# Performance work log

Measured on AMD Instinct MI355X. Metric: run time of the kernel, lower is better.

Reference implementation:

```python
import jax, jax.numpy as jnp
import numpy as np


def setup_inputs() -> dict:
    key = jax.random.key(0)
    ks = jax.random.split(key, 5)
    B, T, C = 2, 2048, 1024
    x = jax.random.normal(ks[0], (B, T, C), dtype=jnp.float32)
    Wqkv = jax.random.normal(ks[1], (C, 3 * C), dtype=jnp.float32) * (C ** -0.5)
    bqkv = jax.random.normal(ks[2], (3 * C,), dtype=jnp.float32) * 0.02
    Wproj = jax.random.normal(ks[3], (C, C), dtype=jnp.float32) * (C ** -0.5)
    bproj = jax.random.normal(ks[4], (C,), dtype=jnp.float32) * 0.02
    return {"x": x, "Wqkv": Wqkv, "bqkv": bqkv, "Wproj": Wproj, "bproj": bproj}


def reference(x, Wqkv, bqkv, Wproj, bproj):
    B, T, C = x.shape
    n_head = 16
    hd = C // n_head
    x_proj = x @ Wqkv + bqkv  # [B, T, 3C]
    # NOTE: source reshapes (B, T, C) -> (B, n_head, T, hd) directly (no transpose);
    # we replicate that exactly for faithfulness.
    q = x_proj[:, :, :C].reshape(B, n_head, T, hd)
    k = x_proj[:, :, C:2 * C].reshape(B, n_head, T, hd)
    v = x_proj[:, :, 2 * C:].reshape(B, n_head, T, hd)
    att = jnp.einsum('bhtd,bhsd->bhts', q, k) * (1.0 / jnp.sqrt(jnp.float32(hd)))
    causal = jnp.tril(jnp.ones((T, T), dtype=bool))  # True where allowed
    att = jnp.where(causal, att, jnp.float32(-jnp.inf))
    att = jax.nn.softmax(att, axis=-1)
    y = att @ v  # [B, H, T, hd]
    y = jnp.transpose(y, (0, 2, 1, 3)).reshape(B, T, C)
    return y @ Wproj + bproj
```

## Files before the change

### kernel.cpp

```cpp
#include <hip/hip_runtime.h>
#include <hip/hip_bf16.h>
#include <stdint.h>

typedef __hip_bfloat16 bf16;
typedef __attribute__((ext_vector_type(8))) short bf16x8;
typedef __attribute__((ext_vector_type(4))) float f32x4;

__device__ __forceinline__ bf16x8 ldsv8(const bf16* p) { return *(const bf16x8*)p; }

__device__ __forceinline__ short bf_bits(float f) {
  union { bf16 h; short s; } u; u.h = __float2bfloat16(f); return u.s;
}

#define ASYNC16(ldsdst, gsrc)                                                  \
  __builtin_amdgcn_global_load_lds(                                            \
      (const __attribute__((address_space(1))) void*)(gsrc),                   \
      (__attribute__((address_space(3))) void*)(ldsdst), 16, 0, 0)

__device__ __forceinline__ bool is_bf16(const void* p) {
  const uint32_t* w = (const uint32_t*)p;
  int cnt = 0;
#pragma unroll 8
  for (int i = 0; i < 64; ++i) {
    uint32_t e = (w[i] >> 7) & 0xffu;
    cnt += (e >= 100u && e <= 150u) ? 1 : 0;
  }
  return cnt >= 40;
}

__device__ __forceinline__ float load_f32(const void* p, size_t idx, bool b16) {
  return b16 ? __bfloat162float(((const bf16*)p)[idx]) : ((const float*)p)[idx];
}

__global__ __launch_bounds__(256) void cvt_k(const float* __restrict__ in,
                                             bf16* __restrict__ out) {
  size_t i = (size_t)blockIdx.x * 256 + threadIdx.x;
  const float4 f0 = ((const float4*)in)[i * 2];
  const float4 f1 = ((const float4*)in)[i * 2 + 1];
  bf16x8 pk = {bf_bits(f0.x), bf_bits(f0.y), bf_bits(f0.z), bf_bits(f0.w),
               bf_bits(f1.x), bf_bits(f1.y), bf_bits(f1.z), bf_bits(f1.w)};
  ((bf16x8*)out)[i] = pk;
}

__global__ __launch_bounds__(256) void cvtT_k(const void* __restrict__ in,
                                              bf16* __restrict__ out,
                                              int R, int Ccols) {
  __shared__ __align__(16) bf16 tile[32][33];
  const bool b16 = is_bf16(in);
  int tx = threadIdx.x & 31, ty = threadIdx.x >> 5;
  int c0 = blockIdx.x * 32, r0 = blockIdx.y * 32;
#pragma unroll
  for (int i = 0; i < 32; i += 8)
    tile[ty + i][tx] = __float2bfloat16(load_f32(in, (size_t)(r0 + ty + i) * Ccols + c0 + tx, b16));
  __syncthreads();
#pragma unroll
  for (int i = 0; i < 32; i += 8)
    out[(size_t)(c0 + ty + i) * R + r0 + tx] = tile[tx][ty + i];
}

template <int MODE>
__global__ __launch_bounds__(256) void gemm128(
    const void* __restrict__ Araw, const bf16* __restrict__ BT,
    const void* __restrict__ biasraw, void* __restrict__ outv) {
  constexpr int K = 1024;
  __shared__ __align__(16) bf16 As[128 * 32];
  __shared__ __align__(16) bf16 Bs[128 * 32];
  const int tid = threadIdx.x;
  const int wave = tid >> 6, lane = tid & 63;
  const int quad = lane >> 4, l16 = lane & 15;
  const int m0 = blockIdx.x * 128, n0 = blockIdx.y * 128;
  const int wm = (wave & 1) * 64, wn = (wave >> 1) * 64;
  const bool a16 = (MODE == 0) ? is_bf16(Araw) : true;
  const bool bias16 = is_bf16(biasraw);

  f32x4 acc[4][4] = {};

  for (int kt = 0; kt < K; kt += 32) {
    __syncthreads();
    if (MODE != 0 || a16) {
#pragma unroll
      for (int i = 0; i < 2; ++i) {
        int slot = i * 256 + tid;
        int row = slot >> 2, col = (slot & 3) << 3;
        ASYNC16(As + slot * 8, ((const bf16*)Araw) + (size_t)(m0 + row) * K + kt + col);
        ASYNC16(Bs + slot * 8, BT + (size_t)(n0 + row) * K + kt + col);
      }
    } else {
#pragma unroll
      for (int i = 0; i < 2; ++i) {
        int slot = i * 256 + tid;
        int row = slot >> 2, col = (slot & 3) << 3;
        const float* ap = ((const float*)Araw) + (size_t)(m0 + row) * K + kt + col;
        float4 f0 = *(const float4*)ap;
        float4 f1 = *(const float4*)(ap + 4);
        bf16x8 pk = {bf_bits(f0.x), bf_bits(f0.y), bf_bits(f0.z), bf_bits(f0.w),
                     bf_bits(f1.x), bf_bits(f1.y), bf_bits(f1.z), bf_bits(f1.w)};
        *(bf16x8*)(As + slot * 8) = pk;
        *(bf16x8*)(Bs + slot * 8) = *(const bf16x8*)(BT + (size_t)(n0 + row) * K + kt + col);
      }
    }
    __syncthreads();
    bf16x8 af[4], bfr[4];
#pragma unroll
    for (int i = 0; i < 4; ++i)
      af[i] = ldsv8(As + (wm + i * 16 + l16) * 32 + quad * 8);
#pragma unroll
    for (int j = 0; j < 4; ++j)
      bfr[j] = ldsv8(Bs + (wn + j * 16 + l16) * 32 + quad * 8);
#pragma unroll
    for (int i = 0; i < 4; ++i)
#pragma unroll
      for (int j = 0; j < 4; ++j)
        acc[i][j] = __builtin_amdgcn_mfma_f32_16x16x32_bf16(af[i], bfr[j], acc[i][j], 0, 0, 0);
  }

  float biasf[4];
#pragma unroll
  for (int j = 0; j < 4; ++j)
    biasf[j] = load_f32(biasraw, n0 + wn + j * 16 + l16, bias16);

#pragma unroll
  for (int i = 0; i < 4; ++i)
#pragma unroll
    for (int j = 0; j < 4; ++j) {
      int ng = n0 + wn + j * 16 + l16;
#pragma unroll
      for (int r = 0; r < 4; ++r) {
        int mg = m0 + wm + i * 16 + quad * 4 + r;
        float v = acc[i][j][r] + biasf[j];
        if (MODE == 1) {
          ((float*)outv)[(size_t)mg * 1024 + ng] = v;
        } else {
          ((bf16*)outv)[(size_t)mg * 3072 + ng] =
              __float2bfloat16(ng < 1024 ? v * 0.125f : v);
        }
      }
    }
}

__global__ __launch_bounds__(512) void attn_k(const bf16* __restrict__ xproj,
                                              bf16* __restrict__ Yb) {
  __shared__ __align__(16) bf16 Ks[128 * 72];
  __shared__ __align__(16) bf16 VTs[64 * 136];
  __shared__ __align__(16) bf16 Ps[8 * 16 * 136];

  const int tid = threadIdx.x;
  const int wave = tid >> 6, lane = tid & 63;
  const int quad = lane >> 4, l16 = lane & 15;
  const int pid = blockIdx.x;
  const int qtA = pid, qtB = 15 - pid;
  const int bh = blockIdx.y, b = bh >> 4, h = bh & 15;
  const size_t rowbase = (size_t)(b * 2048 + h * 128) * 3072;
  const int q0[2] = {qtA * 128, qtB * 128};

  bf16x8 aq[2][2];
#pragma unroll
  for (int t = 0; t < 2; ++t) {
    int sg = q0[t] + wave * 16 + l16;
    const bf16* qp = xproj + rowbase + (size_t)(sg >> 4) * 3072 + ((sg & 15) << 6);
#pragma unroll
    for (int ks = 0; ks < 2; ++ks)
      aq[t][ks] = *(const bf16x8*)(qp + ks * 32 + quad * 8);
  }

  f32x4 o[2][4] = {};
  float mrow[2][4], lrow[2][4];
#pragma unroll
  for (int t = 0; t < 2; ++t)
#pragma unroll
    for (int r = 0; r < 4; ++r) { mrow[t][r] = -1e30f; lrow[t][r] = 0.f; }

  bf16* Pw = Ps + wave * (16 * 136);

  const int slot0 = tid, slot1 = 512 + tid;
  const int sA = slot0 >> 3, blkA = slot0 & 7;
  const int sB = slot1 >> 3, blkB = slot1 & 7;

  bf16x8 kreg[2], vreg[2];
#define ISSUE_LOADS(stv)                                                        \
  {                                                                             \
    int sg0 = (stv)*128 + sA, sg1 = (stv)*128 + sB;                             \
    const bf16* b0 = xproj + rowbase + (size_t)(sg0 >> 4) * 3072 + ((sg0 & 15) << 6); \
    const bf16* b1 = xproj + rowbase + (size_t)(sg1 >> 4) * 3072 + ((sg1 & 15) << 6); \
    kreg[0] = *(const bf16x8*)(b0 + 1024 + blkA * 8);                           \
    vreg[0] = *(const bf16x8*)(b0 + 2048 + blkA * 8);                           \
    kreg[1] = *(const bf16x8*)(b1 + 1024 + blkB * 8);                           \
    vreg[1] = *(const bf16x8*)(b1 + 2048 + blkB * 8);                           \
  }

  ISSUE_LOADS(0);

  for (int st = 0; st <= qtB; ++st) {
    __syncthreads();
    {
      *(bf16x8*)(Ks + sA * 72 + blkA * 8) = kreg[0];
      const bf16* ve0 = (const bf16*)&vreg[0];
      const int ssw0 = sA ^ (blkA << 3);
#pragma unroll
      for (int j = 0; j < 8; ++j) VTs[(blkA * 8 + j) * 136 + ssw0] = ve0[j];
      *(bf16x8*)(Ks + sB * 72 + blkB * 8) = kreg[1];
      const bf16* ve1 = (const bf16*)&vreg[1];
      const int ssw1 = sB ^ (blkB << 3);
#pragma unroll
      for (int j = 0; j < 8; ++j) VTs[(blkB * 8 + j) * 136 + ssw1] = ve1[j];
    }
    if (st < qtB) ISSUE_LOADS(st + 1);
    __syncthreads();

    const bool doA = (st <= qtA);
#pragma unroll
    for (int t = 0; t < 2; ++t) {
      if (t == 0 && !doA) continue;
      const bool diag = (st == (t == 0 ? qtA : qtB));

      f32x4 sc[8] = {};
      __builtin_amdgcn_s_setprio(1);
#pragma unroll
      for (int ks = 0; ks < 2; ++ks)
#pragma unroll
        for (int j = 0; j < 8; ++j) {
          bf16x8 bk = ldsv8(Ks + (j * 16 + l16) * 72 + (ks * 4 + quad) * 8);
          sc[j] = __builtin_amdgcn_mfma_f32_16x16x32_bf16(aq[t][ks], bk, sc[j], 0, 0, 0);
        }
      __builtin_amdgcn_s_setprio(0);

#pragma unroll
      for (int r = 0; r < 4; ++r) {
        const int rloc = wave * 16 + quad * 4 + r;
        float vals[8];
        float mx = -1e30f;
#pragma unroll
        for (int j = 0; j < 8; ++j) {
          float v = sc[j][r];
          if (diag && (j * 16 + l16) > rloc) v = -1e30f;
          vals[j] = v;
          mx = fmaxf(mx, v);
        }
#pragma unroll
        for (int d = 1; d < 16; d <<= 1) mx = fmaxf(mx, __shfl_xor(mx, d, 64));
        float mnew = fmaxf(mrow[t][r], mx);
        float alpha = __expf(mrow[t][r] - mnew);
        mrow[t][r] = mnew;
        float rs = 0.f;
#pragma unroll
        for (int j = 0; j < 8; ++j) {
          float p = __expf(vals[j] - mnew);
          vals[j] = p;
          rs += p;
        }
#pragma unroll
        for (int d = 1; d < 16; d <<= 1) rs += __shfl_xor(rs, d, 64);
        lrow[t][r] = lrow[t][r] * alpha + rs;
#pragma unroll
        for (int j = 0; j < 4; ++j) o[t][j][r] *= alpha;
        bf16* prow = Pw + (quad * 4 + r) * 136;
        const int psw = quad << 3;
#pragma unroll
        for (int j = 0; j < 8; ++j) prow[(j * 16 + l16) ^ psw] = __float2bfloat16(vals[j]);
      }

      __builtin_amdgcn_s_setprio(1);
#pragma unroll
      for (int ks = 0; ks < 4; ++ks) {
        bf16x8 ap = ldsv8(Pw + l16 * 136 + (((ks * 4 + quad) ^ (l16 >> 2)) << 3));
#pragma unroll
        for (int j = 0; j < 4; ++j) {
          int d = j * 16 + l16;
          bf16x8 bv = ldsv8(VTs + d * 136 + (((ks * 4 + quad) ^ (2 * j + (l16 >> 3))) << 3));
          o[t][j] = __builtin_amdgcn_mfma_f32_16x16x32_bf16(ap, bv, o[t][j], 0, 0, 0);
        }
      }
      __builtin_amdgcn_s_setprio(0);
    }
  }
#undef ISSUE_LOADS

  bf16* Yh = Yb + (size_t)b * 2097152 + h * 64;
#pragma unroll
  for (int t = 0; t < 2; ++t)
#pragma unroll
    for (int r = 0; r < 4; ++r) {
      int tt = q0[t] + wave * 16 + quad * 4 + r;
      float inv = 1.f / lrow[t][r];
#pragma unroll
      for (int j = 0; j < 4; ++j)
        Yh[(size_t)tt * 1024 + j * 16 + l16] = __float2bfloat16(o[t][j][r] * inv);
    }
}

extern "C" void kernel_launch(void* const* d_in, const int* in_sizes, int n_in,
                              void* d_out, int out_size, void* d_ws, size_t ws_size,
                              hipStream_t stream) {
  (void)out_size;
  const void* px     = d_in[0];
  const void* pWqkv  = (n_in > 1) ? d_in[1] : d_in[0];
  const void* pbqkv  = (n_in > 2) ? d_in[2] : d_in[0];
  const void* pWproj = (n_in > 3) ? d_in[3] : d_in[0];
  const void* pbproj = (n_in > 4) ? d_in[4] : d_in[0];
  for (int i = 0; i < n_in; ++i) {
    switch (in_sizes[i]) {
      case 4194304: px     = d_in[i]; break;
      case 3145728: pWqkv  = d_in[i]; break;
      case 3072:    pbqkv  = d_in[i]; break;
      case 1048576: pWproj = d_in[i]; break;
      case 1024:    pbproj = d_in[i]; break;
      default: break;
    }
  }

  char* ws = (char*)d_ws;
  bf16* xproj = (bf16*)(ws + 0);

  if (ws_size >= 39845888) {
    bf16* xb     = (bf16*)(ws + 25165824);
    bf16* WqkvT  = (bf16*)(ws + 33554432);
    bf16* WprojT = (bf16*)(ws + 25165824);
    bf16* Yb     = (bf16*)(ws + 27262976);

    cvt_k<<<dim3(2048), 256, 0, stream>>>((const float*)px, xb);
    cvtT_k<<<dim3(96, 32), 256, 0, stream>>>(pWqkv, WqkvT, 1024, 3072);
    gemm128<0><<<dim3(32, 24), 256, 0, stream>>>(xb, WqkvT, pbqkv, xproj);
    cvtT_k<<<dim3(32, 32), 256, 0, stream>>>(pWproj, WprojT, 1024, 1024);
    attn_k<<<dim3(8, 32), 512, 0, stream>>>(xproj, Yb);
    gemm128<1><<<dim3(32, 8), 256, 0, stream>>>(Yb, WprojT, pbproj, d_out);
  } else {
    bf16* WqkvT  = (bf16*)(ws + 25165824);
    bf16* WprojT = (bf16*)(ws + 25165824);
    bf16* Yb     = (bf16*)(ws + 27262976);

    cvtT_k<<<dim3(96, 32), 256, 0, stream>>>(pWqkv, WqkvT, 1024, 3072);
    gemm128<0><<<dim3(32, 24), 256, 0, stream>>>(px, WqkvT, pbqkv, xproj);
    cvtT_k<<<dim3(32, 32), 256, 0, stream>>>(pWproj, WprojT, 1024, 1024);
    attn_k<<<dim3(8, 32), 512, 0, stream>>>(xproj, Yb);
    gemm128<1><<<dim3(32, 8), 256, 0, stream>>>(Yb, WprojT, pbproj, d_out);
  }
}
```

Before: 214.7 us.

## Fuse prep conversions into one launch, narrow proj GEMM tile, skip softmax rescale

Merges the x conversion and both weight transpose-conversions into a single prep kernel, which removes two launches when the workspace is large enough. It adds a BN template parameter so the output projection uses 128x64 tiles, giving 512 blocks instead of 256 for better CU fill. In attention, the causal mask is only applied on diagonal tiles, and the exp-based rescale of o and l is skipped when no row max grew across the wave. This adds a wave-wide vote and branching, plus a new workspace-size path that needs more memory.

```diff
diff --git a/kernel.cpp b/kernel.cpp
--- a/kernel.cpp
+++ b/kernel.cpp
@@ -30,6 +30,52 @@
 
 __device__ __forceinline__ float load_f32(const void* p, size_t idx, bool b16) {
   return b16 ? __bfloat162float(((const bf16*)p)[idx]) : ((const float*)p)[idx];
+}
+
+__device__ __forceinline__ void cvtT_body(const void* in, bf16* out, int R,
+                                          int Ccols, int bx, int by,
+                                          bf16 (*tile)[33]) {
+  const bool b16 = is_bf16(in);
+  int tx = threadIdx.x & 31, ty = threadIdx.x >> 5;
+  int c0 = bx * 32, r0 = by * 32;
+#pragma unroll
+  for (int i = 0; i < 32; i += 8)
+    tile[ty + i][tx] = __float2bfloat16(load_f32(in, (size_t)(r0 + ty + i) * Ccols + c0 + tx, b16));
+  __syncthreads();
+#pragma unroll
+  for (int i = 0; i < 32; i += 8)
+    out[(size_t)(c0 + ty + i) * R + r0 + tx] = tile[tx][ty + i];
+}
+
+__global__ __launch_bounds__(256) void prep_k(const float* __restrict__ x,
+                                              bf16* __restrict__ xb,
+                                              const void* __restrict__ Wqkv,
+                                              bf16* __restrict__ WqkvT,
+                                              const void* __restrict__ Wproj,
+                                              bf16* __restrict__ WprojT) {
+  __shared__ __align__(16) bf16 tile[32][33];
+  const int id = blockIdx.x;
+  if (id < 2048) {
+    size_t i = (size_t)id * 256 + threadIdx.x;
+    const float4 f0 = ((const float4*)x)[i * 2];
+    const float4 f1 = ((const float4*)x)[i * 2 + 1];
+    bf16x8 pk = {bf_bits(f0.x), bf_bits(f0.y), bf_bits(f0.z), bf_bits(f0.w),
+                 bf_bits(f1.x), bf_bits(f1.y), bf_bits(f1.z), bf_bits(f1.w)};
+    ((bf16x8*)xb)[i] = pk;
+  } else if (id < 5120) {
+    int id2 = id - 2048;
+    cvtT_body(Wqkv, WqkvT, 1024, 3072, id2 % 96, id2 / 96, tile);
+  } else {
+    int id3 = id - 5120;
+    cvtT_body(Wproj, WprojT, 1024, 1024, id3 % 32, id3 / 32, tile);
+  }
+}
+
+__global__ __launch_bounds__(256) void cvtT_k(const void* __restrict__ in,
+                                              bf16* __restrict__ out,
+                                              int R, int Ccols) {
+  __shared__ __align__(16) bf16 tile[32][33];
+  cvtT_body(in, out, R, Ccols, blockIdx.x, blockIdx.y, tile);
 }
 
 __global__ __launch_bounds__(256) void cvt_k(const float* __restrict__ in,
@@ -42,38 +88,23 @@
   ((bf16x8*)out)[i] = pk;
 }
 
-__global__ __launch_bounds__(256) void cvtT_k(const void* __restrict__ in,
-                                              bf16* __restrict__ out,
-                                              int R, int Ccols) {
-  __shared__ __align__(16) bf16 tile[32][33];
-  const bool b16 = is_bf16(in);
-  int tx = threadIdx.x & 31, ty = threadIdx.x >> 5;
-  int c0 = blockIdx.x * 32, r0 = blockIdx.y * 32;
-#pragma unroll
-  for (int i = 0; i < 32; i += 8)
-    tile[ty + i][tx] = __float2bfloat16(load_f32(in, (size_t)(r0 + ty + i) * Ccols + c0 + tx, b16));
-  __syncthreads();
-#pragma unroll
-  for (int i = 0; i < 32; i += 8)
-    out[(size_t)(c0 + ty + i) * R + r0 + tx] = tile[tx][ty + i];
-}
-
-template <int MODE>
+template <int MODE, int BN>
 __global__ __launch_bounds__(256) void gemm128(
     const void* __restrict__ Araw, const bf16* __restrict__ BT,
     const void* __restrict__ biasraw, void* __restrict__ outv) {
   constexpr int K = 1024;
+  constexpr int NBF = BN / 32;
   __shared__ __align__(16) bf16 As[128 * 32];
-  __shared__ __align__(16) bf16 Bs[128 * 32];
+  __shared__ __align__(16) bf16 Bs[BN * 32];
   const int tid = threadIdx.x;
   const int wave = tid >> 6, lane = tid & 63;
   const int quad = lane >> 4, l16 = lane & 15;
-  const int m0 = blockIdx.x * 128, n0 = blockIdx.y * 128;
-  const int wm = (wave & 1) * 64, wn = (wave >> 1) * 64;
+  const int m0 = blockIdx.x * 128, n0 = blockIdx.y * BN;
+  const int wm = (wave & 1) * 64, wn = (wave >> 1) * (BN / 2);
   const bool a16 = (MODE == 0) ? is_bf16(Araw) : true;
   const bool bias16 = is_bf16(biasraw);
 
-  f32x4 acc[4][4] = {};
+  f32x4 acc[4][NBF] = {};
 
   for (int kt = 0; kt < K; kt += 32) {
     __syncthreads();
@@ -83,6 +114,11 @@
         int slot = i * 256 + tid;
         int row = slot >> 2, col = (slot & 3) << 3;
         ASYNC16(As + slot * 8, ((const bf16*)Araw) + (size_t)(m0 + row) * K + kt + col);
+      }
+#pragma unroll
+      for (int i = 0; i < BN / 64; ++i) {
+        int slot = i * 256 + tid;
+        int row = slot >> 2, col = (slot & 3) << 3;
         ASYNC16(Bs + slot * 8, BT + (size_t)(n0 + row) * K + kt + col);
       }
     } else {
@@ -96,33 +132,34 @@
         bf16x8 pk = {bf_bits(f0.x), bf_bits(f0.y), bf_bits(f0.z), bf_bits(f0.w),
                      bf_bits(f1.x), bf_bits(f1.y), bf_bits(f1.z), bf_bits(f1.w)};
         *(bf16x8*)(As + slot * 8) = pk;
-        *(bf16x8*)(Bs + slot * 8) = *(const bf16x8*)(BT + (size_t)(n0 + row) * K + kt + col);
+        if (i * 256 < BN * 4)
+          *(bf16x8*)(Bs + slot * 8) = *(const bf16x8*)(BT + (size_t)(n0 + row) * K + kt + col);
       }
     }
     __syncthreads();
-    bf16x8 af[4], bfr[4];
+    bf16x8 af[4], bfr[NBF];
 #pragma unroll
     for (int i = 0; i < 4; ++i)
       af[i] = ldsv8(As + (wm + i * 16 + l16) * 32 + quad * 8);
 #pragma unroll
-    for (int j = 0; j < 4; ++j)
+    for (int j = 0; j < NBF; ++j)
       bfr[j] = ldsv8(Bs + (wn + j * 16 + l16) * 32 + quad * 8);
 #pragma unroll
     for (int i = 0; i < 4; ++i)
 #pragma unroll
-      for (int j = 0; j < 4; ++j)
+      for (int j = 0; j < NBF; ++j)
         acc[i][j] = __builtin_amdgcn_mfma_f32_16x16x32_bf16(af[i], bfr[j], acc[i][j], 0, 0, 0);
   }
 
-  float biasf[4];
-#pragma unroll
-  for (int j = 0; j < 4; ++j)
+  float biasf[NBF];
+#pragma unroll
+  for (int j = 0; j < NBF; ++j)
     biasf[j] = load_f32(biasraw, n0 + wn + j * 16 + l16, bias16);
 
 #pragma unroll
   for (int i = 0; i < 4; ++i)
 #pragma unroll
-    for (int j = 0; j < 4; ++j) {
+    for (int j = 0; j < NBF; ++j) {
       int ng = n0 + wn + j * 16 + l16;
 #pragma unroll
       for (int r = 0; r < 4; ++r) {
@@ -226,21 +263,36 @@
 
 #pragma unroll
       for (int r = 0; r < 4; ++r) {
-        const int rloc = wave * 16 + quad * 4 + r;
         float vals[8];
         float mx = -1e30f;
-#pragma unroll
-        for (int j = 0; j < 8; ++j) {
-          float v = sc[j][r];
-          if (diag && (j * 16 + l16) > rloc) v = -1e30f;
-          vals[j] = v;
-          mx = fmaxf(mx, v);
+        if (diag) {
+          const int rloc = wave * 16 + quad * 4 + r;
+#pragma unroll
+          for (int j = 0; j < 8; ++j) {
+            float v = sc[j][r];
+            if ((j * 16 + l16) > rloc) v = -1e30f;
+            vals[j] = v;
+            mx = fmaxf(mx, v);
+          }
+        } else {
+#pragma unroll
+          for (int j = 0; j < 8; ++j) {
+            float v = sc[j][r];
+            vals[j] = v;
+            mx = fmaxf(mx, v);
+          }
         }
 #pragma unroll
         for (int d = 1; d < 16; d <<= 1) mx = fmaxf(mx, __shfl_xor(mx, d, 64));
-        float mnew = fmaxf(mrow[t][r], mx);
-        float alpha = __expf(mrow[t][r] - mnew);
-        mrow[t][r] = mnew;
+        const bool stable = __all(mx <= mrow[t][r]);
+        float mnew, alpha = 1.0f;
+        if (stable) {
+          mnew = mrow[t][r];
+        } else {
+          mnew = fmaxf(mrow[t][r], mx);
+          alpha = __expf(mrow[t][r] - mnew);
+          mrow[t][r] = mnew;
+        }
         float rs = 0.f;
 #pragma unroll
         for (int j = 0; j < 8; ++j) {
@@ -250,9 +302,13 @@
         }
 #pragma unroll
         for (int d = 1; d < 16; d <<= 1) rs += __shfl_xor(rs, d, 64);
-        lrow[t][r] = lrow[t][r] * alpha + rs;
-#pragma unroll
-        for (int j = 0; j < 4; ++j) o[t][j][r] *= alpha;
+        if (stable) {
+          lrow[t][r] += rs;
+        } else {
+          lrow[t][r] = lrow[t][r] * alpha + rs;
+#pragma unroll
+          for (int j = 0; j < 4; ++j) o[t][j][r] *= alpha;
+        }
         bf16* prow = Pw + (quad * 4 + r) * 136;
         const int psw = quad << 3;
 #pragma unroll
@@ -311,7 +367,18 @@
   char* ws = (char*)d_ws;
   bf16* xproj = (bf16*)(ws + 0);
 
-  if (ws_size >= 39845888) {
+  if (ws_size >= 41943040) {
+    bf16* xb     = (bf16*)(ws + 25165824);
+    bf16* WqkvT  = (bf16*)(ws + 33554432);
+    bf16* WprojT = (bf16*)(ws + 39845888);
+    bf16* Yb     = (bf16*)(ws + 27262976);
+
+    prep_k<<<dim3(6144), 256, 0, stream>>>((const float*)px, xb, pWqkv, WqkvT,
+                                           pWproj, WprojT);
+    gemm128<0, 128><<<dim3(32, 24), 256, 0, stream>>>(xb, WqkvT, pbqkv, xproj);
+    attn_k<<<dim3(8, 32), 512, 0, stream>>>(xproj, Yb);
+    gemm128<1, 64><<<dim3(32, 16), 256, 0, stream>>>(Yb, WprojT, pbproj, d_out);
+  } else if (ws_size >= 39845888) {
     bf16* xb     = (bf16*)(ws + 25165824);
     bf16* WqkvT  = (bf16*)(ws + 33554432);
     bf16* WprojT = (bf16*)(ws + 25165824);
@@ -319,19 +386,19 @@
 
     cvt_k<<<dim3(2048), 256, 0, stream>>>((const float*)px, xb);
     cvtT_k<<<dim3(96, 32), 256, 0, stream>>>(pWqkv, WqkvT, 1024, 3072);
-    gemm128<0><<<dim3(32, 24), 256, 0, stream>>>(xb, WqkvT, pbqkv, xproj);
+    gemm128<0, 128><<<dim3(32, 24), 256, 0, stream>>>(xb, WqkvT, pbqkv, xproj);
     cvtT_k<<<dim3(32, 32), 256, 0, stream>>>(pWproj, WprojT, 1024, 1024);
     attn_k<<<dim3(8, 32), 512, 0, stream>>>(xproj, Yb);
-    gemm128<1><<<dim3(32, 8), 256, 0, stream>>>(Yb, WprojT, pbproj, d_out);
+    gemm128<1, 64><<<dim3(32, 16), 256, 0, stream>>>(Yb, WprojT, pbproj, d_out);
   } else {
     bf16* WqkvT  = (bf16*)(ws + 25165824);
     bf16* WprojT = (bf16*)(ws + 25165824);
     bf16* Yb     = (bf16*)(ws + 27262976);
 
     cvtT_k<<<dim3(96, 32), 256, 0, stream>>>(pWqkv, WqkvT, 1024, 3072);
-    gemm128<0><<<dim3(32, 24), 256, 0, stream>>>(px, WqkvT, pbqkv, xproj);
+    gemm128<0, 128><<<dim3(32, 24), 256, 0, stream>>>(px, WqkvT, pbqkv, xproj);
     cvtT_k<<<dim3(32, 32), 256, 0, stream>>>(pWproj, WprojT, 1024, 1024);
     attn_k<<<dim3(8, 32), 512, 0, stream>>>(xproj, Yb);
-    gemm128<1><<<dim3(32, 8), 256, 0, stream>>>(Yb, WprojT, pbproj, d_out);
-  }
-}
+    gemm128<1, 64><<<dim3(32, 16), 256, 0, stream>>>(Yb, WprojT, pbproj, d_out);
+  }
+}
```

Result: faster. 209.7 us (-2.3%).
